# Kernel tuning notes

Measured on AMD Instinct MI355X. Metric: run time of the kernel, lower is better.

## Reference

```python
import jax, jax.numpy as jnp
import numpy as np

B, N_GENES, N_SETS, G = 256, 10000, 1000, 128   # batch, input_dim, output_dim, geneset_size
H1, H2 = 64, 32                                  # hidden_dims
EPS = 1e-5                                       # BatchNorm1d eps


def _batchnorm(h, gamma, beta):
    # BatchNorm1d in training mode: biased batch stats over the batch axis
    mean = jnp.mean(h, axis=0, keepdims=True)
    var = jnp.mean(jnp.square(h - mean), axis=0, keepdims=True)
    return (h - mean) * jax.lax.rsqrt(var + EPS) * gamma + beta


def setup_inputs() -> dict:
    key = jax.random.key(0)
    ks = jax.random.split(key, 7)
    # Adjacency with exactly G distinct ones per column -> gather index list [N_SETS, G]
    rng = np.random.default_rng(0)
    gene_idx = np.argsort(rng.random((N_SETS, N_GENES)), axis=1)[:, :G]
    gene_idx = jnp.asarray(np.sort(gene_idx, axis=1), dtype=jnp.int32)

    x = jax.random.normal(ks[0], (B, N_GENES), jnp.float32)
    s1, s2, s3 = 1.0 / np.sqrt(G), 1.0 / np.sqrt(H1), 1.0 / np.sqrt(H2)
    W1 = jax.random.uniform(ks[1], (N_SETS, G, H1), jnp.float32, -s1, s1)
    b1 = jax.random.uniform(ks[2], (N_SETS, H1), jnp.float32, -s1, s1)
    W2 = jax.random.uniform(ks[3], (N_SETS, H1, H2), jnp.float32, -s2, s2)
    b2 = jax.random.uniform(ks[4], (N_SETS, H2), jnp.float32, -s2, s2)
    W3 = jax.random.uniform(ks[5], (N_SETS, H2), jnp.float32, -s3, s3)
    b3 = jax.random.uniform(ks[6], (N_SETS,), jnp.float32, -s3, s3)
    g1 = jnp.ones((N_SETS, H1), jnp.float32)
    be1 = jnp.zeros((N_SETS, H1), jnp.float32)
    g2 = jnp.ones((N_SETS, H2), jnp.float32)
    be2 = jnp.zeros((N_SETS, H2), jnp.float32)
    return {"x": x, "gene_idx": gene_idx, "W1": W1, "b1": b1, "g1": g1, "be1": be1,
            "W2": W2, "b2": b2, "g2": g2, "be2": be2, "W3": W3, "b3": b3}


def reference(x, gene_idx, W1, b1, g1, be1, W2, b2, g2, be2, W3, b3):
    # Per-geneset gather: x[:, adj[:,i]==1] for all i at once -> [B, S, G]
    xg = x[:, gene_idx]
    # Linear -> ReLU -> BatchNorm (per geneset, grouped GEMM)
    h = jax.nn.relu(jnp.einsum('bsg,sgh->bsh', xg, W1) + b1)
    h = _batchnorm(h, g1, be1)
    h = jax.nn.relu(jnp.einsum('bsh,shk->bsk', h, W2) + b2)
    h = _batchnorm(h, g2, be2)
    # Final Linear(H2 -> 1) -> ReLU, concatenated over genesets -> [B, S]
    out = jax.nn.relu(jnp.einsum('bsh,sh->bs', h, W3) + b3)
    return out
```

## Files before the change

kernel.cpp:

```cpp
#include <hip/hip_runtime.h>
#include <stdint.h>

#define BB 256
#define NG 10000
#define NS 1000
#define GG 128
#define H1 64
#define H2 32
#define EPSV 1e-5f


typedef unsigned short ushortT;
typedef __attribute__((ext_vector_type(4))) short short4v;
typedef __attribute__((ext_vector_type(8))) short short8v;
typedef __attribute__((ext_vector_type(4))) float float4v;

__device__ __forceinline__ float bf2f(ushortT u) {
    union { uint32_t i; float f; } v; v.i = ((uint32_t)u) << 16; return v.f;
}
__device__ __forceinline__ ushortT f2bf(float f) {
    union { float f; uint32_t i; } v; v.f = f;
    uint32_t x = v.i;
    return (ushortT)((x + 0x7fffu + ((x >> 16) & 1u)) >> 16);
}
__device__ __forceinline__ uint32_t cvtpk_bf16(float lo, float hi) {
    uint32_t d;
    asm("v_cvt_pk_bf16_f32 %0, %1, %2" : "=v"(d) : "v"(lo), "v"(hi));
    return d;
}
__device__ __forceinline__ uint32_t pack2(ushortT lo, ushortT hi) {
    return (uint32_t)lo | ((uint32_t)hi << 16);
}
__device__ __forceinline__ bool probe_f32(const void* g1) {
    return ((*(const uint32_t*)g1) & 0xFFFFu) == 0u;
}
__device__ __forceinline__ float loadf(const void* p, int i, bool isf) {
    return isf ? ((const float*)p)[i] : bf2f(((const ushortT*)p)[i]);
}
__device__ __forceinline__ ushortT loadbf(const void* p, size_t i, bool isf) {
    return isf ? f2bf(((const float*)p)[i]) : ((const ushortT*)p)[i];
}

__global__ __launch_bounds__(256) void k_transpose(const void* __restrict__ x,
                                                   ushortT* __restrict__ xT,
                                                   const void* __restrict__ g1p) {
    __shared__ ushortT tile[64][66];
    const bool isf = probe_f32(g1p);
    const int q = threadIdx.x & 15;
    const int r = threadIdx.x >> 4;
    const int j0 = blockIdx.x * 64;
    const int b0 = blockIdx.y * 64;
    const bool fullj = (j0 + 64 <= NG);
#pragma unroll
    for (int k = 0; k < 4; ++k) {
        const int bl = k * 16 + r;
        const int jq = q * 4;
        const size_t src = (size_t)(b0 + bl) * NG + j0 + jq;
        uint32_t d0, d1;
        if (isf) {
            if (fullj) {
                float4 v = *(const float4*)((const float*)x + src);
                d0 = cvtpk_bf16(v.x, v.y);
                d1 = cvtpk_bf16(v.z, v.w);
            } else {
                float vx[4];
#pragma unroll
                for (int i2 = 0; i2 < 4; ++i2)
                    vx[i2] = (j0 + jq + i2 < NG) ? ((const float*)x)[src + i2] : 0.f;
                d0 = cvtpk_bf16(vx[0], vx[1]);
                d1 = cvtpk_bf16(vx[2], vx[3]);
            }
        } else {
            if (fullj) {
                uint2 v = *(const uint2*)((const ushortT*)x + src);
                d0 = v.x; d1 = v.y;
            } else {
                ushortT e[4];
#pragma unroll
                for (int i2 = 0; i2 < 4; ++i2)
                    e[i2] = (j0 + jq + i2 < NG) ? ((const ushortT*)x)[src + i2] : (ushortT)0;
                d0 = pack2(e[0], e[1]); d1 = pack2(e[2], e[3]);
            }
        }
        *(uint32_t*)(&tile[bl][jq]) = d0;
        *(uint32_t*)(&tile[bl][jq + 2]) = d1;
    }
    __syncthreads();
#pragma unroll
    for (int k = 0; k < 4; ++k) {
        const int jl = k * 16 + r;
        const int jw = j0 + jl;
        if (jw < NG) {
            const int bq = q * 4;
            uint2 o;
            o.x = pack2(tile[bq + 0][jl], tile[bq + 1][jl]);
            o.y = pack2(tile[bq + 2][jl], tile[bq + 3][jl]);
            *(uint2*)(&xT[(size_t)jw * BB + b0 + bq]) = o;
        }
    }
}

__global__ __launch_bounds__(256, 4) void k_main(
    const ushortT* __restrict__ xT, const int* __restrict__ gidx,
    const void* __restrict__ W1, const void* __restrict__ W2,
    const void* __restrict__ b1, const void* __restrict__ g1, const void* __restrict__ be1,
    const void* __restrict__ b2, const void* __restrict__ g2, const void* __restrict__ be2,
    const void* __restrict__ W3, const void* __restrict__ b3,
    void* __restrict__ out) {
    __shared__ ushortT xg[BB * 68];
    __shared__ ushortT w1s[64 * 36];

    char* xgc = (char*)xg;
    ushortT* w2s = w1s;

    const bool isf = probe_f32(g1);
    const int s = blockIdx.x;
    const int t = threadIdx.x;
    const int w = t >> 6;
    const int lane = t & 63;
    const int l16 = lane & 15;
    const int quad = lane >> 4;
    const size_t base1 = (size_t)s * (GG * H1);
    const size_t base2 = (size_t)s * (H1 * H2);

#define HOLE2(r) (*(float2*)(xgc + (r) * 136 + 128))

    const int gq = t & 15;
    const int bo2 = t >> 4;
    const int B0 = bo2 * 16;
    int4 gidA = *(const int4*)(gidx + s * GG + 4 * gq);
    int4 gidB = *(const int4*)(gidx + s * GG + 64 + 4 * gq);

    const float* W1f = (const float*)W1 + base1;
    const ushortT* W1h = (const ushortT*)W1 + base1;

    uint4 w1p[4];
    if (isf) {
        float4 ra[4], rb[4];
#pragma unroll
        for (int q = 0; q < 4; ++q) {
            ra[q] = *(const float4*)(W1f + (size_t)q * 2048 + 8 * t);
            rb[q] = *(const float4*)(W1f + (size_t)q * 2048 + 8 * t + 4);
        }
#pragma unroll
        for (int q = 0; q < 4; ++q) {
            w1p[q].x = cvtpk_bf16(ra[q].x, ra[q].y);
            w1p[q].y = cvtpk_bf16(ra[q].z, ra[q].w);
            w1p[q].z = cvtpk_bf16(rb[q].x, rb[q].y);
            w1p[q].w = cvtpk_bf16(rb[q].z, rb[q].w);
        }
    } else {
#pragma unroll
        for (int q = 0; q < 4; ++q)
            w1p[q] = *(const uint4*)(W1h + (size_t)q * 2048 + 8 * t);
    }

    float b1v[4];
#pragma unroll
    for (int nt = 0; nt < 4; ++nt) b1v[nt] = loadf(b1, s * H1 + nt * 16 + l16, isf);

    auto stageU = [&](uint4 vv) {
        const int g = t >> 3;
        const int h0 = (t & 7) * 8;
        w1s[(h0 + 0) * 36 + g] = (ushortT)vv.x;
        w1s[(h0 + 1) * 36 + g] = (ushortT)(vv.x >> 16);
        w1s[(h0 + 2) * 36 + g] = (ushortT)vv.y;
        w1s[(h0 + 3) * 36 + g] = (ushortT)(vv.y >> 16);
        w1s[(h0 + 4) * 36 + g] = (ushortT)vv.z;
        w1s[(h0 + 5) * 36 + g] = (ushortT)(vv.z >> 16);
        w1s[(h0 + 6) * 36 + g] = (ushortT)vv.w;
        w1s[(h0 + 7) * 36 + g] = (ushortT)(vv.w >> 16);
    };

    float4v acc1[4][4];
#pragma unroll
    for (int mt = 0; mt < 4; ++mt)
#pragma unroll
        for (int nt = 0; nt < 4; ++nt) acc1[mt][nt] = (float4v){0.f, 0.f, 0.f, 0.f};

    uint4 gv[8];
    auto gload = [&](const int4 g4) {
        const ushortT* r0 = xT + (size_t)g4.x * BB + B0;
        const ushortT* r1 = xT + (size_t)g4.y * BB + B0;
        const ushortT* r2 = xT + (size_t)g4.z * BB + B0;
        const ushortT* r3 = xT + (size_t)g4.w * BB + B0;
        gv[0] = *(const uint4*)(r0); gv[1] = *(const uint4*)(r0 + 8);
        gv[2] = *(const uint4*)(r1); gv[3] = *(const uint4*)(r1 + 8);
        gv[4] = *(const uint4*)(r2); gv[5] = *(const uint4*)(r2 + 8);
        gv[6] = *(const uint4*)(r3); gv[7] = *(const uint4*)(r3 + 8);
    };
    auto unpack = [&]() {
#pragma unroll
        for (int oc = 0; oc < 2; ++oc) {
            const uint32_t aw[4] = {gv[0 + oc].x, gv[0 + oc].y, gv[0 + oc].z, gv[0 + oc].w};
            const uint32_t bw[4] = {gv[2 + oc].x, gv[2 + oc].y, gv[2 + oc].z, gv[2 + oc].w};
            const uint32_t cw[4] = {gv[4 + oc].x, gv[4 + oc].y, gv[4 + oc].z, gv[4 + oc].w};
            const uint32_t dw[4] = {gv[6 + oc].x, gv[6 + oc].y, gv[6 + oc].z, gv[6 + oc].w};
#pragma unroll
            for (int p = 0; p < 4; ++p) {
#pragma unroll
                for (int hf = 0; hf < 2; ++hf) {
                    const uint32_t sel = hf ? 0x07060302u : 0x05040100u;
                    uint2 o;
                    o.x = __builtin_amdgcn_perm(bw[p], aw[p], sel);
                    o.y = __builtin_amdgcn_perm(dw[p], cw[p], sel);
                    const int b = B0 + oc * 8 + p * 2 + hf;
                    *(uint2*)(&xg[b * 68 + 4 * gq]) = o;
                }
            }
        }
    };
    auto mfmaChunk = [&](int kt) {
        short8v bfrag[4];
#pragma unroll
        for (int nt = 0; nt < 4; ++nt) {
            const int h = nt * 16 + l16;
            const int woff = h * 36 + quad * 8;
            short4v blo = *(const short4v*)(&w1s[woff]);
            short4v bhi = *(const short4v*)(&w1s[woff + 4]);
            bfrag[nt] = __builtin_shufflevector(blo, bhi, 0, 1, 2, 3, 4, 5, 6, 7);
        }
#pragma unroll
        for (int mt = 0; mt < 4; ++mt) {
            const int b = w * 64 + mt * 16 + l16;
            const ushortT* p = &xg[b * 68 + kt * 32 + quad * 8];
            short4v alo = *(const short4v*)(p);
            short4v ahi = *(const short4v*)(p + 4);
            short8v af = __builtin_shufflevector(alo, ahi, 0, 1, 2, 3, 4, 5, 6, 7);
#pragma unroll
            for (int nt = 0; nt < 4; ++nt)
                acc1[mt][nt] = __builtin_amdgcn_mfma_f32_16x16x32_bf16(af, bfrag[nt], acc1[mt][nt], 0, 0, 0);
        }
    };

    gload(gidA);
    unpack();
    stageU(w1p[0]);
    __syncthreads();
    mfmaChunk(0);
    __syncthreads();
    gload(gidB);
    stageU(w1p[1]);
    __syncthreads();
    mfmaChunk(1);
    unpack();

    float4 w2fa, w2fb; uint4 w2u;
    if (isf) {
        w2fa = *(const float4*)((const float*)W2 + base2 + 8 * t);
        w2fb = *(const float4*)((const float*)W2 + base2 + 8 * t + 4);
    } else {
        w2u = *(const uint4*)((const ushortT*)W2 + base2 + 8 * t);
    }

    __syncthreads();
    stageU(w1p[2]);
    __syncthreads();
    mfmaChunk(0);
    __syncthreads();
    stageU(w1p[3]);
    __syncthreads();
    mfmaChunk(1);

    if (isf) {
        w2u.x = cvtpk_bf16(w2fa.x, w2fa.y);
        w2u.y = cvtpk_bf16(w2fa.z, w2fa.w);
        w2u.z = cvtpk_bf16(w2fb.x, w2fb.y);
        w2u.w = cvtpk_bf16(w2fb.z, w2fb.w);
    }
    float g1a[4], be1a[4];
#pragma unroll
    for (int nt = 0; nt < 4; ++nt) {
        g1a[nt] = loadf(g1, s * H1 + nt * 16 + l16, isf);
        be1a[nt] = loadf(be1, s * H1 + nt * 16 + l16, isf);
    }
    float b2v[2], w3v[2], g2a[2], be2a[2];
#pragma unroll
    for (int nt = 0; nt < 2; ++nt) {
        b2v[nt] = loadf(b2, s * H2 + nt * 16 + l16, isf);
        w3v[nt] = loadf(W3, s * H2 + nt * 16 + l16, isf);
        g2a[nt] = loadf(g2, s * H2 + nt * 16 + l16, isf);
        be2a[nt] = loadf(be2, s * H2 + nt * 16 + l16, isf);
    }
    const float b3v = loadf(b3, s, isf);

#pragma unroll
    for (int nt = 0; nt < 4; ++nt) {
        float s1 = 0.f, s2 = 0.f;
        const float bb = b1v[nt];
#pragma unroll
        for (int mt = 0; mt < 4; ++mt)
#pragma unroll
            for (int r = 0; r < 4; ++r) {
                float v = acc1[mt][nt][r] + bb;
                v = v > 0.f ? v : 0.f;
                s1 += v;
                s2 += v * v;
            }
        s1 += __shfl_xor(s1, 16); s1 += __shfl_xor(s1, 32);
        s2 += __shfl_xor(s2, 16); s2 += __shfl_xor(s2, 32);
        if (lane < 16) HOLE2(w * 64 + nt * 16 + lane) = (float2){s1, s2};
    }
    __syncthreads();

    {
        const int h2 = t >> 2, k0 = (t & 3) * 8;
        w2s[(k0 + 0) * 72 + h2] = (ushortT)w2u.x;
        w2s[(k0 + 1) * 72 + h2] = (ushortT)(w2u.x >> 16);
        w2s[(k0 + 2) * 72 + h2] = (ushortT)w2u.y;
        w2s[(k0 + 3) * 72 + h2] = (ushortT)(w2u.y >> 16);
        w2s[(k0 + 4) * 72 + h2] = (ushortT)w2u.z;
        w2s[(k0 + 5) * 72 + h2] = (ushortT)(w2u.z >> 16);
        w2s[(k0 + 6) * 72 + h2] = (ushortT)w2u.w;
        w2s[(k0 + 7) * 72 + h2] = (ushortT)(w2u.w >> 16);
    }
#pragma unroll
    for (int nt = 0; nt < 4; ++nt) {
        const int h = nt * 16 + l16;
        float ts = 0.f, tq = 0.f;
#pragma unroll
        for (int wv = 0; wv < 4; ++wv) {
            float2 p = HOLE2(h + 64 * wv);
            ts += p.x; tq += p.y;
        }
        float mean = ts * (1.0f / 256.0f);
        float var = tq * (1.0f / 256.0f) - mean * mean;
        var = var > 0.f ? var : 0.f;
        float rs = rsqrtf(var + EPSV);
        const float a = g1a[nt] * rs;
        const float cc = be1a[nt] - mean * a;
        const float bb = b1v[nt];
#pragma unroll
        for (int mt = 0; mt < 4; ++mt) {
            const int b0r = w * 64 + mt * 16 + quad * 4;
#pragma unroll
            for (int rp = 0; rp < 2; ++rp) {
                float v0 = acc1[mt][nt][2 * rp] + bb;     v0 = v0 > 0.f ? v0 : 0.f;
                float v1 = acc1[mt][nt][2 * rp + 1] + bb; v1 = v1 > 0.f ? v1 : 0.f;
                const uint32_t pk = cvtpk_bf16(v0 * a + cc, v1 * a + cc);
                xg[(b0r + 2 * rp) * 68 + h] = (ushortT)pk;
                xg[(b0r + 2 * rp + 1) * 68 + h] = (ushortT)(pk >> 16);
            }
        }
    }
    __syncthreads();

    float4v acc2[4][2];
#pragma unroll
    for (int mt = 0; mt < 4; ++mt)
#pragma unroll
        for (int nt = 0; nt < 2; ++nt) acc2[mt][nt] = (float4v){0.f, 0.f, 0.f, 0.f};

#pragma unroll
    for (int kt = 0; kt < 2; ++kt) {
        const int kl = kt * 32 + quad * 8;
        short8v bfrag2[2];
#pragma unroll
        for (int nt = 0; nt < 2; ++nt) {
            const int k2 = nt * 16 + l16;
            const int woff = k2 * 72 + kl;
            short4v blo = *(const short4v*)(&w2s[woff]);
            short4v bhi = *(const short4v*)(&w2s[woff + 4]);
            bfrag2[nt] = __builtin_shufflevector(blo, bhi, 0, 1, 2, 3, 4, 5, 6, 7);
        }
#pragma unroll
        for (int mt = 0; mt < 4; ++mt) {
            const int b = w * 64 + mt * 16 + l16;
            const ushortT* p = &xg[b * 68 + kl];
            short4v alo = *(const short4v*)(p);
            short4v ahi = *(const short4v*)(p + 4);
            short8v af = __builtin_shufflevector(alo, ahi, 0, 1, 2, 3, 4, 5, 6, 7);
#pragma unroll
            for (int nt = 0; nt < 2; ++nt)
                acc2[mt][nt] = __builtin_amdgcn_mfma_f32_16x16x32_bf16(af, bfrag2[nt], acc2[mt][nt], 0, 0, 0);
        }
    }

#pragma unroll
    for (int nt = 0; nt < 2; ++nt) {
        float s1 = 0.f, s2 = 0.f;
        const float bb = b2v[nt];
#pragma unroll
        for (int mt = 0; mt < 4; ++mt)
#pragma unroll
            for (int r = 0; r < 4; ++r) {
                float v = acc2[mt][nt][r] + bb;
                v = v > 0.f ? v : 0.f;
                s1 += v;
                s2 += v * v;
            }
        s1 += __shfl_xor(s1, 16); s1 += __shfl_xor(s1, 32);
        s2 += __shfl_xor(s2, 16); s2 += __shfl_xor(s2, 32);
        if (lane < 16) HOLE2(w * 32 + nt * 16 + lane) = (float2){s1, s2};
    }
    __syncthreads();

    float a2[2], c2[2];
#pragma unroll
    for (int nt = 0; nt < 2; ++nt) {
        const int k2 = nt * 16 + l16;
        float ts = 0.f, tq = 0.f;
#pragma unroll
        for (int wv = 0; wv < 4; ++wv) {
            float2 p = HOLE2(k2 + 32 * wv);
            ts += p.x; tq += p.y;
        }
        float mean = ts * (1.0f / 256.0f);
        float var = tq * (1.0f / 256.0f) - mean * mean;
        var = var > 0.f ? var : 0.f;
        float rs = rsqrtf(var + EPSV);
        a2[nt] = g2a[nt] * rs;
        c2[nt] = be2a[nt] - mean * a2[nt];
    }
#pragma unroll
    for (int mt = 0; mt < 4; ++mt)
#pragma unroll
        for (int r = 0; r < 4; ++r) {
            float tot = 0.f;
#pragma unroll
            for (int nt = 0; nt < 2; ++nt) {
                float v = acc2[mt][nt][r] + b2v[nt];
                v = v > 0.f ? v : 0.f;
                tot += (v * a2[nt] + c2[nt]) * w3v[nt];
            }
            tot += __shfl_xor(tot, 1);
            tot += __shfl_xor(tot, 2);
            tot += __shfl_xor(tot, 4);
            tot += __shfl_xor(tot, 8);
            if (l16 == 0) {
                const int b = w * 64 + mt * 16 + quad * 4 + r;
                float o = tot + b3v;
                o = o > 0.f ? o : 0.f;
                if (isf) ((float*)out)[b * NS + s] = o;
                else     ((ushortT*)out)[b * NS + s] = f2bf(o);
            }
        }
#undef HOLE2
}

extern "C" void kernel_launch(void* const* d_in, const int* in_sizes, int n_in,
                              void* d_out, int out_size, void* d_ws, size_t ws_size,
                              hipStream_t stream) {
    const int* gi = (const int*)d_in[1];
    ushortT* xT = (ushortT*)d_ws;

    dim3 gT((NG + 63) / 64, BB / 64);
    k_transpose<<<gT, 256, 0, stream>>>(d_in[0], xT, d_in[4]);
    k_main<<<NS, 256, 0, stream>>>(xT, gi, d_in[2], d_in[6],
                                   d_in[3], d_in[4], d_in[5],
                                   d_in[7], d_in[8], d_in[9], d_in[10], d_in[11],
                                   d_out);
}
```

Before: 149.6 us.

## Stream W1 quarters in a double-buffered pipeline instead of preloading all

Instead of loading all four quarters of W1 into registers up front, the kernel loads one quarter ahead of use and converts f32 to bf16 at staging time (stageF), overlapping each next load with the current MFMA chunk. This cuts the register pressure from holding 16 float4s and spreads global loads across compute phases. The gidB load and the second gather are also reordered. The risk is exposing load latency if the prefetch distance is too short.

```diff
diff --git a/kernel.cpp b/kernel.cpp
--- a/kernel.cpp
+++ b/kernel.cpp
@@ -129,36 +129,34 @@
     const int bo2 = t >> 4;
     const int B0 = bo2 * 16;
     int4 gidA = *(const int4*)(gidx + s * GG + 4 * gq);
-    int4 gidB = *(const int4*)(gidx + s * GG + 64 + 4 * gq);
 
     const float* W1f = (const float*)W1 + base1;
     const ushortT* W1h = (const ushortT*)W1 + base1;
 
-    uint4 w1p[4];
-    if (isf) {
-        float4 ra[4], rb[4];
-#pragma unroll
-        for (int q = 0; q < 4; ++q) {
-            ra[q] = *(const float4*)(W1f + (size_t)q * 2048 + 8 * t);
-            rb[q] = *(const float4*)(W1f + (size_t)q * 2048 + 8 * t + 4);
-        }
-#pragma unroll
-        for (int q = 0; q < 4; ++q) {
-            w1p[q].x = cvtpk_bf16(ra[q].x, ra[q].y);
-            w1p[q].y = cvtpk_bf16(ra[q].z, ra[q].w);
-            w1p[q].z = cvtpk_bf16(rb[q].x, rb[q].y);
-            w1p[q].w = cvtpk_bf16(rb[q].z, rb[q].w);
-        }
+    uint4 w1A0, w1A1, w1B0, w1B1;
+    if (isf) {
+        w1A0 = *(const uint4*)(W1f + (size_t)(0 * 512 + 0 * 256 + t) * 4);
+        w1A1 = *(const uint4*)(W1f + (size_t)(0 * 512 + 1 * 256 + t) * 4);
     } else {
-#pragma unroll
-        for (int q = 0; q < 4; ++q)
-            w1p[q] = *(const uint4*)(W1h + (size_t)q * 2048 + 8 * t);
+        w1A0 = *(const uint4*)(W1h + (size_t)0 * 2048 + t * 8);
     }
 
     float b1v[4];
 #pragma unroll
     for (int nt = 0; nt < 4; ++nt) b1v[nt] = loadf(b1, s * H1 + nt * 16 + l16, isf);
 
+    auto stageF = [&](uint4 vv, int rr) {
+        union { uint32_t i; float f; } u0, u1, u2, u3;
+        u0.i = vv.x; u1.i = vv.y; u2.i = vv.z; u3.i = vv.w;
+        const int g = rr * 16 + (t >> 4);
+        const int h0 = (t & 15) * 4;
+        const uint32_t p01 = cvtpk_bf16(u0.f, u1.f);
+        const uint32_t p23 = cvtpk_bf16(u2.f, u3.f);
+        w1s[(h0 + 0) * 36 + g] = (ushortT)p01;
+        w1s[(h0 + 1) * 36 + g] = (ushortT)(p01 >> 16);
+        w1s[(h0 + 2) * 36 + g] = (ushortT)p23;
+        w1s[(h0 + 3) * 36 + g] = (ushortT)(p23 >> 16);
+    };
     auto stageU = [&](uint4 vv) {
         const int g = t >> 3;
         const int h0 = (t & 7) * 8;
@@ -235,16 +233,30 @@
 
     gload(gidA);
     unpack();
-    stageU(w1p[0]);
+    int4 gidB = *(const int4*)(gidx + s * GG + 64 + 4 * gq);
+    if (isf) { stageF(w1A0, 0); stageF(w1A1, 1); } else { stageU(w1A0); }
+    if (isf) {
+        w1B0 = *(const uint4*)(W1f + (size_t)(1 * 512 + 0 * 256 + t) * 4);
+        w1B1 = *(const uint4*)(W1f + (size_t)(1 * 512 + 1 * 256 + t) * 4);
+    } else {
+        w1B0 = *(const uint4*)(W1h + (size_t)1 * 2048 + t * 8);
+    }
     __syncthreads();
     mfmaChunk(0);
     __syncthreads();
+    if (isf) { stageF(w1B0, 0); stageF(w1B1, 1); } else { stageU(w1B0); }
+    if (isf) {
+        w1A0 = *(const uint4*)(W1f + (size_t)(2 * 512 + 0 * 256 + t) * 4);
+        w1A1 = *(const uint4*)(W1f + (size_t)(2 * 512 + 1 * 256 + t) * 4);
+    } else {
+        w1A0 = *(const uint4*)(W1h + (size_t)2 * 2048 + t * 8);
+    }
+    __syncthreads();
+    mfmaChunk(1);
+
     gload(gidB);
-    stageU(w1p[1]);
-    __syncthreads();
-    mfmaChunk(1);
+    __syncthreads();
     unpack();
-
     float4 w2fa, w2fb; uint4 w2u;
     if (isf) {
         w2fa = *(const float4*)((const float*)W2 + base2 + 8 * t);
@@ -252,13 +264,17 @@
     } else {
         w2u = *(const uint4*)((const ushortT*)W2 + base2 + 8 * t);
     }
-
-    __syncthreads();
-    stageU(w1p[2]);
+    if (isf) { stageF(w1A0, 0); stageF(w1A1, 1); } else { stageU(w1A0); }
+    if (isf) {
+        w1B0 = *(const uint4*)(W1f + (size_t)(3 * 512 + 0 * 256 + t) * 4);
+        w1B1 = *(const uint4*)(W1f + (size_t)(3 * 512 + 1 * 256 + t) * 4);
+    } else {
+        w1B0 = *(const uint4*)(W1h + (size_t)3 * 2048 + t * 8);
+    }
     __syncthreads();
     mfmaChunk(0);
     __syncthreads();
-    stageU(w1p[3]);
+    if (isf) { stageF(w1B0, 0); stageF(w1B1, 1); } else { stageU(w1B0); }
     __syncthreads();
     mfmaChunk(1);
 
```

Result: faster. 145.8 us (-2.5%).
